# Kernel tuning notes

Hardware: AMD Instinct MI355X
Metric: run time of the kernel (lower is better)

The kernel has to match this reference:

```python
import jax, jax.numpy as jnp
import numpy as np

B, P, M, C = 8192, 8, 2048, 1024


def setup_inputs() -> dict:
    key = jax.random.key(0)
    k1, k2 = jax.random.split(key)
    stdv = 1.0 / np.sqrt(C)
    inp = jax.random.normal(k1, (B, C), dtype=jnp.float32)
    weight = jax.random.uniform(k2, (P, M, C), dtype=jnp.float32, minval=-stdv, maxval=stdv)
    return {"input": inp, "weight": weight}


def reference(input, weight):
    # scores: [B, P, M] = <input_c, weight_pmc>
    att = jnp.einsum('bc,pmc->bpm', input, weight)
    att = jax.nn.softmax(att, axis=2)
    # combine with the same memory bank as values: [B, P, C]
    out = jnp.einsum('bpm,pmc->bpc', att, weight)
    return out
```

## Files before the change

### kernel.cpp

```cpp
#include <hip/hip_runtime.h>
#include <hip/hip_bf16.h>
#include <cstdint>
#include <cstddef>

#define B_SZ 8192
#define P_SZ 8
#define M_SZ 2048
#define C_SZ 1024

using bfrag = __attribute__((ext_vector_type(8))) short;
using facc  = __attribute__((ext_vector_type(4))) float;
using u16x4 = __attribute__((ext_vector_type(4))) unsigned short;

typedef __attribute__((address_space(1))) const void g_void;
typedef __attribute__((address_space(3))) void l_void;

__device__ __forceinline__ unsigned short f2bf(float x) {
    union { __hip_bfloat16 h; unsigned short u; } cv;
    cv.h = __float2bfloat16(x);
    return cv.u;
}
__device__ __forceinline__ float bf2f(unsigned short u) {
    union { unsigned int i; float f; } cv;
    cv.i = ((unsigned int)u) << 16;
    return cv.f;
}

#define WAIT_LGKM0() do { asm volatile("s_waitcnt lgkmcnt(0)" ::: "memory"); \
                          __builtin_amdgcn_sched_barrier(0); } while (0)
#define WAIT_VM(n)   do { asm volatile("s_waitcnt vmcnt(" #n ")" ::: "memory"); \
                          __builtin_amdgcn_sched_barrier(0); } while (0)
#define S_BARRIER()     asm volatile("s_barrier" ::: "memory")
#define LGKM0_BARRIER() asm volatile("s_waitcnt lgkmcnt(0)\n\ts_barrier" ::: "memory")
#define WAIT_VM_RAW(n)  asm volatile("s_waitcnt vmcnt(" #n ")" ::: "memory")

__global__ void cvt_q_kernel(const float* __restrict__ in, unsigned short* __restrict__ q) {
    const size_t i = (size_t)blockIdx.x * blockDim.x + threadIdx.x;
    const float4 v = ((const float4*)in)[i];
    u16x4 o = { f2bf(v.x), f2bf(v.y), f2bf(v.z), f2bf(v.w) };
    ((u16x4*)q)[i] = o;
}

__global__ void cvt_w_kernel(const float* __restrict__ w,
                             unsigned short* __restrict__ wb,
                             unsigned short* __restrict__ wt) {
    __shared__ float t[32][33];
    const int bid = blockIdx.x;
    const int p  = bid >> 11;
    const int m0 = ((bid >> 5) & 63) << 5;
    const int c0 = (bid & 31) << 5;
    const int tx = threadIdx.x & 7;
    const int ty = threadIdx.x >> 3;
    const float4 v = *(const float4*)(w + ((size_t)p*M_SZ + m0 + ty)*C_SZ + c0 + tx*4);
    u16x4 o = { f2bf(v.x), f2bf(v.y), f2bf(v.z), f2bf(v.w) };
    *(u16x4*)(wb + ((size_t)p*M_SZ + m0 + ty)*C_SZ + c0 + tx*4) = o;
    t[ty][tx*4+0] = v.x; t[ty][tx*4+1] = v.y; t[ty][tx*4+2] = v.z; t[ty][tx*4+3] = v.w;
    __syncthreads();
    float4 u2;
    u2.x = t[tx*4+0][ty]; u2.y = t[tx*4+1][ty]; u2.z = t[tx*4+2][ty]; u2.w = t[tx*4+3][ty];
    u16x4 o2 = { f2bf(u2.x), f2bf(u2.y), f2bf(u2.z), f2bf(u2.w) };
    *(u16x4*)(wt + ((size_t)p*C_SZ + c0 + ty)*M_SZ + m0 + tx*4) = o2;
}

constexpr int GLDS = 131072;

template<int KLEN>
__device__ __forceinline__ void stage_half8(const unsigned short* panelBase, char* ldsOp,
                                            int hh, int kt, int tid) {
    #pragma unroll
    for (int i = 0; i < 2; ++i) {
        const int o  = i*8192 + tid*16;
        const int rl = o >> 7;
        const int r  = hh*128 + rl;
        const int ps = (o >> 4) & 7;
        const int ls = ps ^ (r & 7);
        const unsigned short* src = panelBase + (size_t)r*KLEN + kt*64 + ls*8;
        char* dst = ldsOp + hh*16384 + i*8192 + ((tid >> 6) << 10);
        __builtin_amdgcn_global_load_lds((g_void*)src, (l_void*)dst, 16, 0, 0);
    }
}

__device__ __forceinline__ void loadA8(const char* ldsAbuf, int qm, int wm, int l15, int g,
                                       bfrag (&aF)[4][2]) {
    #pragma unroll
    for (int mf = 0; mf < 4; ++mf) {
        const int r = qm*128 + wm*64 + mf*16 + l15;
        const char* rp = ldsAbuf + r*128;
        #pragma unroll
        for (int ks = 0; ks < 2; ++ks)
            aF[mf][ks] = *(const bfrag*)(rp + (((ks*4 + g) ^ (r & 7)) << 4));
    }
}

__device__ __forceinline__ void loadB8(const char* ldsBbuf, int qn, int wn, int l15, int g,
                                       bfrag (&bF)[2][2]) {
    #pragma unroll
    for (int nf = 0; nf < 2; ++nf) {
        const int r = qn*128 + wn*32 + nf*16 + l15;
        const char* rp = ldsBbuf + r*128;
        #pragma unroll
        for (int ks = 0; ks < 2; ++ks)
            bF[nf][ks] = *(const bfrag*)(rp + (((ks*4 + g) ^ (r & 7)) << 4));
    }
}

template<int QM, int QN, int MODE, int DOSUM>
__device__ __forceinline__ void mfma_phase(const bfrag (&aF)[4][2], const bfrag (&bF)[2][2],
                                           facc (&acc)[8][4], float (&rs)[8]) {
    __builtin_amdgcn_s_setprio(1);
    #pragma unroll
    for (int ks = 0; ks < 2; ++ks)
        #pragma unroll
        for (int mf = 0; mf < 4; ++mf)
            #pragma unroll
            for (int nf = 0; nf < 2; ++nf)
                acc[QM*4 + mf][QN*2 + nf] = __builtin_amdgcn_mfma_f32_16x16x32_bf16(
                    aF[mf][ks], bF[nf][ks], acc[QM*4 + mf][QN*2 + nf], 0, 0, 0);
    if (MODE == 1 && DOSUM) {
        #pragma unroll
        for (int mf = 0; mf < 4; ++mf)
            #pragma unroll
            for (int ks = 0; ks < 2; ++ks)
                #pragma unroll
                for (int e = 0; e < 8; ++e)
                    rs[QM*4 + mf] += bf2f((unsigned short)aF[mf][ks][e]);
    }
    __builtin_amdgcn_s_setprio(0);
}

template<int KLEN, int NTN, int MODE>
__global__ __launch_bounds__(512, 2)
void gemm8(const unsigned short* __restrict__ A,
           const unsigned short* __restrict__ Bm,
           unsigned short* __restrict__ Pout,
           float* __restrict__ Oout,
           size_t APS, size_t BPS)
{
    extern __shared__ char lds[];
    const int tid  = threadIdx.x;
    const int lane = tid & 63;
    const int wid  = tid >> 6;
    const int wm   = wid >> 2;
    const int wn   = wid & 3;
    const int g    = lane >> 4;
    const int l15  = lane & 15;

    const int p       = blockIdx.x & 7;
    const int logical = blockIdx.x >> 3;
    const int nt      = logical % NTN;
    const int mt      = logical / NTN;

    const unsigned short* Abase = A  + (size_t)p*APS + (size_t)mt*256*KLEN;
    const unsigned short* Bbase = Bm + (size_t)p*BPS + (size_t)nt*256*KLEN;

    facc acc[8][4];
    #pragma unroll
    for (int i = 0; i < 8; ++i)
        #pragma unroll
        for (int j = 0; j < 4; ++j) acc[i][j] = facc{0.f, 0.f, 0.f, 0.f};
    float rs[8] = {0.f,0.f,0.f,0.f,0.f,0.f,0.f,0.f};

    constexpr int NKT = KLEN / 64;

    stage_half8<KLEN>(Bbase, lds + 32768,         0, 0, tid);
    stage_half8<KLEN>(Abase, lds + 0,             0, 0, tid);
    stage_half8<KLEN>(Bbase, lds + 32768,         1, 0, tid);
    stage_half8<KLEN>(Abase, lds + 0,             1, 0, tid);
    stage_half8<KLEN>(Abase, lds + 65536,         0, (1 < NKT ? 1 : NKT-1), tid);
    stage_half8<KLEN>(Bbase, lds + 65536 + 32768, 1, (1 < NKT ? 1 : NKT-1), tid);
    WAIT_VM(4);
    __builtin_amdgcn_s_barrier();

    bfrag aF[4][2], bLow[2][2], bHigh[2][2];

    for (int t = 0; t < NKT; ++t) {
        const int cur = t & 1;
        char* ldsA  = lds + cur*65536;
        char* ldsB  = ldsA + 32768;
        char* ldsAn = lds + (cur^1)*65536;
        char* ldsBn = ldsAn + 32768;
        const int t1 = (t+1 < NKT) ? t+1 : NKT-1;
        const int t2 = (t+2 < NKT) ? t+2 : NKT-1;

        loadA8(ldsA, 0, wm, l15, g, aF);
        loadB8(ldsB, 0, wn, l15, g, bLow);
        stage_half8<KLEN>(Bbase, ldsBn, 0, t1, tid);
        __builtin_amdgcn_s_barrier();
        WAIT_LGKM0();
        mfma_phase<0,0,MODE,1>(aF, bLow, acc, rs);
        __builtin_amdgcn_s_barrier();

        loadB8(ldsB, 1, wn, l15, g, bHigh);
        stage_half8<KLEN>(Abase, ldsAn, 1, t1, tid);
        __builtin_amdgcn_s_barrier();
        WAIT_LGKM0();
        mfma_phase<0,1,MODE,0>(aF, bHigh, acc, rs);
        __builtin_amdgcn_s_barrier();

        loadA8(ldsA, 1, wm, l15, g, aF);
        stage_half8<KLEN>(Abase, ldsA, 0, t2, tid);
        __builtin_amdgcn_s_barrier();
        WAIT_LGKM0();
        mfma_phase<1,1,MODE,1>(aF, bHigh, acc, rs);
        __builtin_amdgcn_s_barrier();

        stage_half8<KLEN>(Bbase, ldsB, 1, t2, tid);
        __builtin_amdgcn_s_barrier();
        mfma_phase<1,0,MODE,0>(aF, bLow, acc, rs);
        WAIT_VM(4);
        __builtin_amdgcn_s_barrier();
    }

    const int row0g = mt*256;
    const int col0g = nt*256;
    __syncthreads();

    if (MODE == 0) {
        unsigned short* Pp = Pout + (size_t)p * ((size_t)B_SZ * M_SZ);
        unsigned short* plds = (unsigned short*)lds;
        #pragma unroll
        for (int c2 = 0; c2 < 2; ++c2) {
            #pragma unroll
            for (int mf = 0; mf < 4; ++mf)
                #pragma unroll
                for (int j = 0; j < 4; ++j) {
                    const int r = wm*64 + mf*16 + g*4 + j;
                    #pragma unroll
                    for (int qn = 0; qn < 2; ++qn)
                        #pragma unroll
                        for (int nf = 0; nf < 2; ++nf)
                            plds[r*256 + qn*128 + wn*32 + nf*16 + l15] =
                                f2bf(__expf(acc[c2*4+mf][qn*2+nf][j]));
                }
            WAIT_LGKM0();
            __builtin_amdgcn_s_barrier();
            #pragma unroll
            for (int i = 0; i < 8; ++i) {
                const int o  = i*8192 + tid*16;
                const int r  = o >> 9;
                const int cb = o & 511;
                *(bfrag*)((char*)(Pp + (size_t)(row0g + c2*128 + r)*M_SZ + col0g) + cb) =
                    *(const bfrag*)((char*)plds + o);
            }
            WAIT_LGKM0();
            __builtin_amdgcn_s_barrier();
        }
    } else {
        float* flds = (float*)lds;
        #pragma unroll
        for (int c2 = 0; c2 < 4; ++c2) {
            const int qm = c2 >> 1;
            if (wm == (c2 & 1)) {
                #pragma unroll
                for (int mf = 0; mf < 4; ++mf) {
                    float d = rs[qm*4 + mf];
                    d += __shfl_xor(d, 16);
                    d += __shfl_xor(d, 32);
                    #pragma unroll
                    for (int j = 0; j < 4; ++j) {
                        const float inv = 1.0f / __shfl(d, g*4 + j);
                        const int r = mf*16 + g*4 + j;
                        #pragma unroll
                        for (int qn = 0; qn < 2; ++qn)
                            #pragma unroll
                            for (int nf = 0; nf < 2; ++nf)
                                flds[r*256 + qn*128 + wn*32 + nf*16 + l15] =
                                    acc[qm*4+mf][qn*2+nf][j] * inv;
                    }
                }
            }
            WAIT_LGKM0();
            __builtin_amdgcn_s_barrier();
            #pragma unroll
            for (int i = 0; i < 8; ++i) {
                const int o  = i*8192 + tid*16;
                const int r  = o >> 10;
                const int cb = o & 1023;
                *(float4*)((char*)(Oout + ((size_t)(row0g + c2*64 + r)*P_SZ + p)*C_SZ + col0g) + cb) =
                    *(const float4*)((char*)flds + o);
            }
            WAIT_LGKM0();
            __builtin_amdgcn_s_barrier();
        }
    }
}

template<int KLEN, int NTN, int CPX, int MODE>
__global__ __launch_bounds__(256, 2)
void gemm_tile(const unsigned short* __restrict__ A,
               const unsigned short* __restrict__ Bm,
               unsigned short* __restrict__ Pout,
               float* __restrict__ Oout,
               int p)
{
    __shared__ alignas(16) char lds[32768];
    const int tid  = threadIdx.x;
    const int lane = tid & 63;
    const int wid  = tid >> 6;
    const int wr   = wid >> 1;
    const int wc   = wid & 1;
    const int g    = lane >> 4;
    const int l15  = lane & 15;

    const int logical = (blockIdx.x & 7) * CPX + (blockIdx.x >> 3);
    const int mt = logical / NTN;
    const int nt = logical % NTN;

    const unsigned short* Abase = A  + (size_t)mt * 128 * KLEN;
    const unsigned short* Bbase = Bm + (size_t)nt * 128 * KLEN;

    facc acc[4][4];
    #pragma unroll
    for (int i = 0; i < 4; ++i)
        #pragma unroll
        for (int j = 0; j < 4; ++j) acc[i][j] = facc{0.f, 0.f, 0.f, 0.f};
    float rs[4] = {0.f, 0.f, 0.f, 0.f};

    constexpr int NKT = KLEN / 32;

    auto stage = [&](int kt) {
        char* buf = lds + (kt & 1) * 16384;
        const unsigned short* As = Abase + kt * 32;
        const unsigned short* Bs = Bbase + kt * 32;
        #pragma unroll
        for (int i = 0; i < 2; ++i) {
            const int o  = i * 4096 + tid * 16;
            const int r  = o >> 6;
            const int s  = (o >> 4) & 3;
            const int cs = s ^ ((r >> 1) & 3);
            __builtin_amdgcn_global_load_lds((g_void*)(As + (size_t)r * KLEN + cs * 8),
                                             (l_void*)(buf + i * 4096 + ((tid >> 6) << 10)),
                                             16, 0, 0);
        }
        #pragma unroll
        for (int i = 0; i < 2; ++i) {
            const int o  = i * 4096 + tid * 16;
            const int r  = o >> 6;
            const int s  = (o >> 4) & 3;
            const int cs = s ^ ((r >> 1) & 3);
            __builtin_amdgcn_global_load_lds((g_void*)(Bs + (size_t)r * KLEN + cs * 8),
                                             (l_void*)(buf + 8192 + i * 4096 + ((tid >> 6) << 10)),
                                             16, 0, 0);
        }
    };

    stage(0);
    stage(1);

    const int cb = ((((l15 >> 1) & 3) ^ g) << 4);

    for (int kt = 0; kt < NKT; ++kt) {
        if (kt + 1 < NKT) { WAIT_VM_RAW(4); } else { WAIT_VM_RAW(0); }
        S_BARRIER();
        const char* Ab = lds + (kt & 1) * 16384;
        const char* Bb = Ab + 8192;
        bfrag af[4], bb[4];
        #pragma unroll
        for (int mf = 0; mf < 4; ++mf)
            af[mf] = *(const bfrag*)(Ab + (wr * 64 + mf * 16 + l15) * 64 + cb);
        #pragma unroll
        for (int nf = 0; nf < 4; ++nf)
            bb[nf] = *(const bfrag*)(Bb + (wc * 64 + nf * 16 + l15) * 64 + cb);
        LGKM0_BARRIER();
        if (kt + 2 < NKT) stage(kt + 2);
        if (MODE == 1) {
            #pragma unroll
            for (int mf = 0; mf < 4; ++mf)
                #pragma unroll
                for (int e = 0; e < 8; ++e)
                    rs[mf] += bf2f((unsigned short)af[mf][e]);
        }
        #pragma unroll
        for (int mf = 0; mf < 4; ++mf)
            #pragma unroll
            for (int nf = 0; nf < 4; ++nf)
                acc[mf][nf] = __builtin_amdgcn_mfma_f32_16x16x32_bf16(af[mf], bb[nf], acc[mf][nf], 0, 0, 0);
    }

    if (MODE == 0) {
        const int prow0 = mt * 128 + wr * 64;
        const int pcol0 = nt * 128 + wc * 64;
        #pragma unroll
        for (int mf = 0; mf < 4; ++mf)
            #pragma unroll
            for (int j = 0; j < 4; ++j) {
                const size_t rbase = (size_t)(prow0 + mf * 16 + g * 4 + j) * M_SZ + pcol0 + l15;
                #pragma unroll
                for (int nf = 0; nf < 4; ++nf)
                    Pout[rbase + nf * 16] = f2bf(__expf(acc[mf][nf][j]));
            }
    } else {
        const int orow0 = mt * 128 + wr * 64;
        const int ocol0 = nt * 128 + wc * 64;
        #pragma unroll
        for (int mf = 0; mf < 4; ++mf) {
            float d = rs[mf];
            d += __shfl_xor(d, 16);
            d += __shfl_xor(d, 32);
            #pragma unroll
            for (int j = 0; j < 4; ++j) {
                const float inv = 1.0f / __shfl(d, g * 4 + j);
                const size_t rbase = ((size_t)(orow0 + mf * 16 + g * 4 + j) * P_SZ + p) * C_SZ
                                   + ocol0 + l15;
                #pragma unroll
                for (int nf = 0; nf < 4; ++nf)
                    Oout[rbase + nf * 16] = acc[mf][nf][j] * inv;
            }
        }
    }
}

__global__ void emu_fallback(const float* __restrict__ inF, const float* __restrict__ wF,
                             float* __restrict__ out)
{
    __shared__ float sc[M_SZ];
    __shared__ float qs[C_SZ];
    __shared__ float wsum[4];
    const int b = blockIdx.x;
    const int tid = threadIdx.x;
    for (int c = tid; c < C_SZ; c += 256) qs[c] = inF[(size_t)b*C_SZ + c];
    __syncthreads();
    for (int p = 0; p < P_SZ; ++p) {
        const float* wp = wF + (size_t)p*M_SZ*C_SZ;
        for (int m = tid; m < M_SZ; m += 256) {
            float d = 0.f;
            const float* wr = wp + (size_t)m*C_SZ;
            for (int c = 0; c < C_SZ; ++c) d += qs[c]*wr[c];
            sc[m] = __expf(d);
        }
        __syncthreads();
        float part = 0.f;
        for (int m = tid; m < M_SZ; m += 256) part += sc[m];
        #pragma unroll
        for (int sft = 1; sft < 64; sft <<= 1) part += __shfl_xor(part, sft);
        if ((tid & 63) == 0) wsum[tid >> 6] = part;
        __syncthreads();
        const float rin = 1.0f / (wsum[0] + wsum[1] + wsum[2] + wsum[3]);
        float o0=0,o1=0,o2=0,o3=0;
        for (int m = 0; m < M_SZ; ++m) {
            const float pm = sc[m];
            const float4 w4 = *(const float4*)(wp + (size_t)m*C_SZ + tid*4);
            o0 += pm*w4.x; o1 += pm*w4.y; o2 += pm*w4.z; o3 += pm*w4.w;
        }
        float* op = out + ((size_t)b*P_SZ + p)*C_SZ + tid*4;
        op[0]=o0*rin; op[1]=o1*rin; op[2]=o2*rin; op[3]=o3*rin;
        __syncthreads();
    }
}

extern "C" void kernel_launch(void* const* d_in, const int* in_sizes, int n_in,
                              void* d_out, int out_size, void* d_ws, size_t ws_size,
                              hipStream_t stream)
{
    (void)in_sizes; (void)n_in; (void)out_size;
    const float* inF = (const float*)d_in[0];
    const float* wF  = (const float*)d_in[1];
    float* out = (float*)d_out;

    const size_t wbE  = (size_t)P_SZ * M_SZ * C_SZ;
    const size_t qE   = (size_t)B_SZ * C_SZ;
    const size_t pME  = (size_t)B_SZ * M_SZ;
    const size_t pAll = pME * P_SZ;
    const size_t needBig   = (wbE*2 + qE + pAll) * sizeof(unsigned short);
    const size_t needMid   = (wbE*2 + qE + pME)  * sizeof(unsigned short);

    if (ws_size >= needBig) {
        unsigned short* wb = (unsigned short*)d_ws;
        unsigned short* wt = wb + wbE;
        unsigned short* qb = wt + wbE;
        unsigned short* Pb = qb + qE;
        cvt_q_kernel<<<(unsigned)(qE/4/256), 256, 0, stream>>>(inF, qb);
        cvt_w_kernel<<<P_SZ*64*32, 256, 0, stream>>>(wF, wb, wt);
        hipFuncSetAttribute(reinterpret_cast<const void*>(&gemm8<C_SZ, 8, 0>),
                            hipFuncAttributeMaxDynamicSharedMemorySize, GLDS);
        gemm8<C_SZ, 8, 0><<<2048, 512, GLDS, stream>>>(
            qb, wb, Pb, nullptr, (size_t)0, (size_t)M_SZ * C_SZ);
        hipFuncSetAttribute(reinterpret_cast<const void*>(&gemm8<M_SZ, 4, 1>),
                            hipFuncAttributeMaxDynamicSharedMemorySize, GLDS);
        gemm8<M_SZ, 4, 1><<<1024, 512, GLDS, stream>>>(
            Pb, wt, nullptr, out, (size_t)B_SZ * M_SZ, (size_t)C_SZ * M_SZ);
    } else if (ws_size >= needMid) {
        unsigned short* wb = (unsigned short*)d_ws;
        unsigned short* wt = wb + wbE;
        unsigned short* qb = wt + wbE;
        unsigned short* Pb = qb + qE;
        cvt_q_kernel<<<(unsigned)(qE/4/256), 256, 0, stream>>>(inF, qb);
        cvt_w_kernel<<<P_SZ*64*32, 256, 0, stream>>>(wF, wb, wt);
        for (int p = 0; p < P_SZ; ++p) {
            gemm_tile<C_SZ, 16, 128, 0><<<1024, 256, 0, stream>>>(
                qb, wb + (size_t)p*M_SZ*C_SZ, Pb, nullptr, p);
            gemm_tile<M_SZ, 8, 64, 1><<<512, 256, 0, stream>>>(
                Pb, wt + (size_t)p*C_SZ*M_SZ, nullptr, out, p);
        }
    } else {
        emu_fallback<<<B_SZ, 256, 0, stream>>>(inF, wF, out);
    }
}
```

Before: 640.5 us.

## Process heads in pairs to shrink intermediate P buffer to L2/MALL scale

Splits the two fused GEMM launches (scores+exp, then weighted sum) into four rounds of two heads each, reusing a P workspace sized for two heads instead of eight. The aim is a smaller bf16 probability intermediate that can stay resident in the large last-level cache between the producer and consumer kernels, cutting HBM traffic. The cost is more kernel launches with fewer blocks each (512 and 256 blocks), which may underfill the GPU and add launch gaps.

```diff
diff --git a/kernel.cpp b/kernel.cpp
--- a/kernel.cpp
+++ b/kernel.cpp
@@ -128,13 +128,13 @@
     __builtin_amdgcn_s_setprio(0);
 }
 
-template<int KLEN, int NTN, int MODE>
+template<int KLEN, int NTN, int MODE, int NP>
 __global__ __launch_bounds__(512, 2)
 void gemm8(const unsigned short* __restrict__ A,
            const unsigned short* __restrict__ Bm,
            unsigned short* __restrict__ Pout,
            float* __restrict__ Oout,
-           size_t APS, size_t BPS)
+           size_t APS, size_t BPS, int p_base)
 {
     extern __shared__ char lds[];
     const int tid  = threadIdx.x;
@@ -145,13 +145,14 @@
     const int g    = lane >> 4;
     const int l15  = lane & 15;
 
-    const int p       = blockIdx.x & 7;
-    const int logical = blockIdx.x >> 3;
-    const int nt      = logical % NTN;
-    const int mt      = logical / NTN;
-
-    const unsigned short* Abase = A  + (size_t)p*APS + (size_t)mt*256*KLEN;
-    const unsigned short* Bbase = Bm + (size_t)p*BPS + (size_t)nt*256*KLEN;
+    constexpr int LNP = (NP == 1) ? 0 : (NP == 2) ? 1 : 2;
+    const int p_loc = blockIdx.x & (NP - 1);
+    const int idx   = ((int)blockIdx.x >> 3) * (8 >> LNP) + ((blockIdx.x & 7) >> LNP);
+    const int nt    = idx % NTN;
+    const int mt    = idx / NTN;
+
+    const unsigned short* Abase = A  + (size_t)p_loc*APS + (size_t)mt*256*KLEN;
+    const unsigned short* Bbase = Bm + (size_t)p_loc*BPS + (size_t)nt*256*KLEN;
 
     facc acc[8][4];
     #pragma unroll
@@ -216,7 +217,7 @@
     __syncthreads();
 
     if (MODE == 0) {
-        unsigned short* Pp = Pout + (size_t)p * ((size_t)B_SZ * M_SZ);
+        unsigned short* Pp = Pout + (size_t)p_loc * ((size_t)B_SZ * M_SZ);
         unsigned short* plds = (unsigned short*)lds;
         #pragma unroll
         for (int c2 = 0; c2 < 2; ++c2) {
@@ -246,6 +247,7 @@
             __builtin_amdgcn_s_barrier();
         }
     } else {
+        const int p_glob = p_base + p_loc;
         float* flds = (float*)lds;
         #pragma unroll
         for (int c2 = 0; c2 < 4; ++c2) {
@@ -276,7 +278,7 @@
                 const int o  = i*8192 + tid*16;
                 const int r  = o >> 10;
                 const int cb = o & 1023;
-                *(float4*)((char*)(Oout + ((size_t)(row0g + c2*64 + r)*P_SZ + p)*C_SZ + col0g) + cb) =
+                *(float4*)((char*)(Oout + ((size_t)(row0g + c2*64 + r)*P_SZ + p_glob)*C_SZ + col0g) + cb) =
                     *(const float4*)((char*)flds + o);
             }
             WAIT_LGKM0();
@@ -460,9 +462,9 @@
     const size_t wbE  = (size_t)P_SZ * M_SZ * C_SZ;
     const size_t qE   = (size_t)B_SZ * C_SZ;
     const size_t pME  = (size_t)B_SZ * M_SZ;
-    const size_t pAll = pME * P_SZ;
-    const size_t needBig   = (wbE*2 + qE + pAll) * sizeof(unsigned short);
-    const size_t needMid   = (wbE*2 + qE + pME)  * sizeof(unsigned short);
+    const size_t p2E  = pME * 2;
+    const size_t needBig = (wbE*2 + qE + p2E) * sizeof(unsigned short);
+    const size_t needMid = (wbE*2 + qE + pME) * sizeof(unsigned short);
 
     if (ws_size >= needBig) {
         unsigned short* wb = (unsigned short*)d_ws;
@@ -471,14 +473,18 @@
         unsigned short* Pb = qb + qE;
         cvt_q_kernel<<<(unsigned)(qE/4/256), 256, 0, stream>>>(inF, qb);
         cvt_w_kernel<<<P_SZ*64*32, 256, 0, stream>>>(wF, wb, wt);
-        hipFuncSetAttribute(reinterpret_cast<const void*>(&gemm8<C_SZ, 8, 0>),
+        hipFuncSetAttribute(reinterpret_cast<const void*>(&gemm8<C_SZ, 8, 0, 2>),
                             hipFuncAttributeMaxDynamicSharedMemorySize, GLDS);
-        gemm8<C_SZ, 8, 0><<<2048, 512, GLDS, stream>>>(
-            qb, wb, Pb, nullptr, (size_t)0, (size_t)M_SZ * C_SZ);
-        hipFuncSetAttribute(reinterpret_cast<const void*>(&gemm8<M_SZ, 4, 1>),
+        hipFuncSetAttribute(reinterpret_cast<const void*>(&gemm8<M_SZ, 4, 1, 2>),
                             hipFuncAttributeMaxDynamicSharedMemorySize, GLDS);
-        gemm8<M_SZ, 4, 1><<<1024, 512, GLDS, stream>>>(
-            Pb, wt, nullptr, out, (size_t)B_SZ * M_SZ, (size_t)C_SZ * M_SZ);
+        for (int pb = 0; pb < P_SZ; pb += 2) {
+            gemm8<C_SZ, 8, 0, 2><<<512, 512, GLDS, stream>>>(
+                qb, wb + (size_t)pb*M_SZ*C_SZ, Pb, nullptr,
+                (size_t)0, (size_t)M_SZ * C_SZ, pb);
+            gemm8<M_SZ, 4, 1, 2><<<256, 512, GLDS, stream>>>(
+                Pb, wt + (size_t)pb*C_SZ*M_SZ, nullptr, out,
+                (size_t)B_SZ * M_SZ, (size_t)C_SZ * M_SZ, pb);
+        }
     } else if (ws_size >= needMid) {
         unsigned short* wb = (unsigned short*)d_ws;
         unsigned short* wt = wb + wbE;
```

New measurement: 685.2 us. 7.0% more time.
